# Kernel tuning notes

Hardware: AMD Instinct MI355X
Metric: run time of the kernel (lower is better)

## Reference

```python
import jax, jax.numpy as jnp
import numpy as np

EPS = 1e-8


def setup_inputs() -> dict:
    key = jax.random.key(0)
    k1, k2, k3, k4 = jax.random.split(key, 4)
    N, Cin, Cout, S, DHW, K = 4, 64, 64, 512, 48, 3
    return {
        "x": jax.random.normal(k1, (N, Cin, DHW, DHW, DHW), dtype=jnp.float32),
        "s": jax.random.normal(k2, (N, S), dtype=jnp.float32),
        "style_weight": jax.random.normal(k3, (Cin, S), dtype=jnp.float32) * (1.0 / np.sqrt(S)),
        "style_bias": jnp.ones((Cin,), dtype=jnp.float32),
        "weight": jax.random.normal(k4, (Cout, Cin, K, K, K), dtype=jnp.float32) * (1.0 / np.sqrt(Cin * K**3)),
        "bias": jnp.zeros((Cout,), dtype=jnp.float32),
    }


def reference(x, s, style_weight, style_bias, weight, bias):
    N, Cin = x.shape[0], x.shape[1]
    Cout = weight.shape[0]
    # style modulation: per-sample per-input-channel scale
    style = s @ style_weight.T + style_bias                      # [N, Cin]
    w = weight[None] * style[:, None, :, None, None, None]       # [N, Cout, Cin, k, k, k]
    # demodulation over fan-in dims (Cin, k, k, k)
    w = w * jax.lax.rsqrt(jnp.sum(w * w, axis=(2, 3, 4, 5), keepdims=True) + EPS)
    w = w.reshape(N * Cout, Cin, *w.shape[3:])                   # grouped kernel
    xg = x.reshape(1, N * Cin, *x.shape[2:])
    y = jax.lax.conv_general_dilated(
        xg, w,
        window_strides=(1, 1, 1),
        padding='VALID',
        feature_group_count=N,
        dimension_numbers=('NCDHW', 'OIDHW', 'NCDHW'),
    )                                                            # [1, N*Cout, D', H', W']
    y = y.reshape(N, Cout, *y.shape[2:])
    return y + bias[None, :, None, None, None]
```

## Files before the change

kernel.cpp:

```cpp
#include <hip/hip_runtime.h>

typedef float f32x4 __attribute__((ext_vector_type(4)));
typedef short bf16x8 __attribute__((ext_vector_type(8)));

#define AS1 __attribute__((address_space(1)))
#define AS3 __attribute__((address_space(3)))

__device__ __forceinline__ void gl16(const void* g, void* l) {
  __builtin_amdgcn_global_load_lds((const AS1 unsigned int*)g,
                                   (AS3 unsigned int*)l, 16, 0, 0);
}

__device__ __forceinline__ unsigned short f2bf(float f) {
  unsigned u = __float_as_uint(f);
  u = u + 0x7FFFu + ((u >> 16) & 1u);
  return (unsigned short)(u >> 16);
}

__global__ __launch_bounds__(256) void k_style(const float* __restrict__ s,
                                               const float* __restrict__ sw,
                                               const float* __restrict__ sb,
                                               float* __restrict__ style) {
  int t = threadIdx.x;
  int n = t >> 6, i = t & 63;
  float acc = sb[i];
  const float* sp = s + n * 512;
  const float* wp = sw + i * 512;
  for (int k = 0; k < 512; ++k) acc += sp[k] * wp[k];
  style[t] = acc;
}

__global__ __launch_bounds__(256) void k_wmod(const float* __restrict__ weight,
                                              const float* __restrict__ style,
                                              unsigned short* __restrict__ wm) {
  int o = blockIdx.x, n = blockIdx.y, t = threadIdx.x;
  int lane = t & 63, wv = t >> 6;
  const float* wp = weight + o * 1728;
  const float* st = style + n * 64;
  float v[7];
  float ss = 0.f;
#pragma unroll
  for (int j = 0; j < 7; ++j) {
    int idx = t + j * 256;
    float w = 0.f;
    if (idx < 1728) {
      int i = idx / 27;
      w = wp[idx] * st[i];
    }
    v[j] = w;
    ss += w * w;
  }
#pragma unroll
  for (int off = 32; off > 0; off >>= 1) ss += __shfl_down(ss, off);
  __shared__ float red[4];
  if (lane == 0) red[wv] = ss;
  __syncthreads();
  float total = red[0] + red[1] + red[2] + red[3];
  float dm = 1.0f / sqrtf(total + 1e-8f);
#pragma unroll
  for (int j = 0; j < 7; ++j) {
    int idx = t + j * 256;
    if (idx < 1728) {
      int i = idx / 27, k = idx - i * 27;
      int g = (n * 27 + k) * 64 + o;
      wm[g * 64 + (((i >> 3) ^ (o & 7)) << 3) + (i & 7)] = f2bf(v[j] * dm);
    }
  }
}

__global__ __launch_bounds__(256) void k_xpose(const float* __restrict__ x,
                                               unsigned short* __restrict__ xT) {
  __shared__ unsigned tile[128][33];
  int n = blockIdx.y;
  int p0 = blockIdx.x * 128;
  int t = threadIdx.x;
  int wv = t >> 6, lane = t & 63;
  const float* xb = x + (size_t)n * 64 * 110592 + p0;
#pragma unroll
  for (int c = 0; c < 8; ++c) {
    int i2 = c * 4 + wv;
    int i = i2 * 2;
    int pl = lane * 2;
    const float* r0 = xb + (size_t)i * 110592 + pl;
    const float* r1 = r0 + 110592;
    float2 a = *(const float2*)r0;
    float2 b = *(const float2*)r1;
    tile[pl][i2]     = (unsigned)f2bf(a.x) | ((unsigned)f2bf(b.x) << 16);
    tile[pl + 1][i2] = (unsigned)f2bf(a.y) | ((unsigned)f2bf(b.y) << 16);
  }
  __syncthreads();
  uint4* dst = (uint4*)xT;
#pragma unroll
  for (int c = 0; c < 4; ++c) {
    int pl = (t >> 3) + c * 32;
    int r = t & 7;
    uint4 u;
    u.x = tile[pl][r * 4 + 0];
    u.y = tile[pl][r * 4 + 1];
    u.z = tile[pl][r * 4 + 2];
    u.w = tile[pl][r * 4 + 3];
    int R = n * 110592 + p0 + pl;
    dst[(size_t)R * 8 + (r ^ (pl & 7))] = u;
  }
}

__global__ __launch_bounds__(256) void k_conv(const unsigned short* __restrict__ xT,
                                              const unsigned short* __restrict__ wm,
                                              const float* __restrict__ bias,
                                              float* __restrict__ out) {
  __shared__ uint4 Bl4[46080 / 16];
  __shared__ uint4 Al4[2][8192 / 16];
  char* Bl = (char*)Bl4;

  int bid = blockIdx.x;
  int orig = (bid & 7) * 207 + (bid >> 3);
  int n = orig / 414;
  int pb = orig - n * 414;
  int p0 = pb * 256;

  int t = threadIdx.x;
  int lane = t & 63, wv = t >> 6;
  int l15 = lane & 15, lhi = lane >> 4;
  f32x4 acc[4][4] = {};

  const char* xb = (const char*)xT + ((size_t)(n * 110592 + p0)) * 128;
  const char* wb = (const char*)wm + (size_t)n * 27 * 8192;

  {
    const char* ap = wb;
    gl16(ap + wv * 1024 + lane * 16, (char*)Al4[0] + wv * 1024);
    gl16(ap + (wv + 4) * 1024 + lane * 16, (char*)Al4[0] + (wv + 4) * 1024);
  }

#pragma unroll
  for (int kd = 0; kd < 3; ++kd) {
    const char* src = xb + (size_t)kd * (2304 * 128);
    for (int cc = wv; cc < 45; cc += 4)
      gl16(src + cc * 1024 + lane * 16, Bl + cc * 1024);
    asm volatile("s_waitcnt vmcnt(0)" ::: "memory");
    __builtin_amdgcn_s_barrier();
    __builtin_amdgcn_sched_barrier(0);

#pragma unroll
    for (int tap = 0; tap < 9; ++tap) {
      const int s = kd * 9 + tap;
      const int cur = s & 1;
      if (s + 1 < 27) {
        const char* ap = wb + (size_t)(s + 1) * 8192;
        gl16(ap + wv * 1024 + lane * 16, (char*)Al4[cur ^ 1] + wv * 1024);
        gl16(ap + (wv + 4) * 1024 + lane * 16, (char*)Al4[cur ^ 1] + (wv + 4) * 1024);
      }
      const int kh = tap / 3, kw = tap - kh * 3;
      const int rbase = wv * 64 + kh * 48 + kw;
      const char* Alc = (const char*)Al4[cur];
#pragma unroll
      for (int ih = 0; ih < 2; ++ih) {
        int c = lhi + ih * 4;
        bf16x8 a[4], b[4];
#pragma unroll
        for (int m = 0; m < 4; ++m) {
          int orow = m * 16 + l15;
          a[m] = *(const bf16x8*)(Alc + orow * 128 + ((c ^ (orow & 7)) << 4));
        }
#pragma unroll
        for (int q = 0; q < 4; ++q) {
          int r = rbase + q * 16 + l15;
          b[q] = *(const bf16x8*)(Bl + r * 128 + ((c ^ (r & 7)) << 4));
        }
        __builtin_amdgcn_s_setprio(1);
#pragma unroll
        for (int m = 0; m < 4; ++m)
#pragma unroll
          for (int q = 0; q < 4; ++q)
            acc[m][q] = __builtin_amdgcn_mfma_f32_16x16x32_bf16(a[m], b[q], acc[m][q], 0, 0, 0);
        __builtin_amdgcn_s_setprio(0);
      }
      asm volatile("s_waitcnt vmcnt(0)" ::: "memory");
      __builtin_amdgcn_s_barrier();
      __builtin_amdgcn_sched_barrier(0);
    }
  }

  float bv[4][4];
#pragma unroll
  for (int m = 0; m < 4; ++m)
#pragma unroll
    for (int r = 0; r < 4; ++r) bv[m][r] = bias[m * 16 + lhi * 4 + r];

  float* ob = out + (size_t)n * 64 * 97336;
#pragma unroll
  for (int q = 0; q < 4; ++q) {
    int p = p0 + wv * 64 + q * 16 + l15;
    int d = p / 2304;
    int rem = p - d * 2304;
    int h = rem / 48;
    int w = rem - h * 48;
    if (h < 46 && w < 46) {
      int base = d * 2116 + h * 46 + w;
#pragma unroll
      for (int m = 0; m < 4; ++m)
#pragma unroll
        for (int r = 0; r < 4; ++r) {
          int o = m * 16 + lhi * 4 + r;
          ob[(size_t)o * 97336 + base] = acc[m][q][r] + bv[m][r];
        }
    }
  }
}

extern "C" void kernel_launch(void* const* d_in, const int* in_sizes, int n_in,
                              void* d_out, int out_size, void* d_ws, size_t ws_size,
                              hipStream_t stream) {
  const float* x    = (const float*)d_in[0];
  const float* s    = (const float*)d_in[1];
  const float* sw   = (const float*)d_in[2];
  const float* sb   = (const float*)d_in[3];
  const float* wt   = (const float*)d_in[4];
  const float* bias = (const float*)d_in[5];
  float* out = (float*)d_out;

  float* style          = (float*)d_ws;
  unsigned short* wm    = (unsigned short*)((char*)d_ws + 1024);
  unsigned short* xT    = (unsigned short*)((char*)d_ws + 1024 + 884736);

  hipLaunchKernelGGL(k_style, dim3(1), dim3(256), 0, stream, s, sw, sb, style);
  hipLaunchKernelGGL(k_wmod, dim3(64, 4), dim3(256), 0, stream, wt, style, wm);
  hipLaunchKernelGGL(k_xpose, dim3(864, 4), dim3(256), 0, stream, x, xT);
  hipLaunchKernelGGL(k_conv, dim3(1656), dim3(256), 0, stream, xT, wm, bias, out);
}
```

Measured before the change: 154.8 us.

## Load modulated weights directly into registers, dropping LDS staging and per-tap barriers

The per-tap weight tile is no longer staged through double-buffered LDS with global_load_lds. Each lane now loads its A fragments straight from global memory into registers, with a register ping-pong between aA and aB. This removes 27 per-tap waitcnt plus barrier pairs, keeping only the barriers around each kd input-slab reload, and frees 16KB of LDS. In exchange it adds about 64 VGPRs for the two A register sets and issues global loads with little latency hiding beyond one tap ahead, which may cut occupancy or stall on global latency.

```diff
diff --git a/kernel.cpp b/kernel.cpp
--- a/kernel.cpp
+++ b/kernel.cpp
@@ -109,7 +109,6 @@
                                               const float* __restrict__ bias,
                                               float* __restrict__ out) {
   __shared__ uint4 Bl4[46080 / 16];
-  __shared__ uint4 Al4[2][8192 / 16];
   char* Bl = (char*)Bl4;
 
   int bid = blockIdx.x;
@@ -126,60 +125,63 @@
   const char* xb = (const char*)xT + ((size_t)(n * 110592 + p0)) * 128;
   const char* wb = (const char*)wm + (size_t)n * 27 * 8192;
 
-  {
-    const char* ap = wb;
-    gl16(ap + wv * 1024 + lane * 16, (char*)Al4[0] + wv * 1024);
-    gl16(ap + (wv + 4) * 1024 + lane * 16, (char*)Al4[0] + (wv + 4) * 1024);
-  }
+  int aoff[8];
+#pragma unroll
+  for (int m = 0; m < 4; ++m)
+#pragma unroll
+    for (int ih = 0; ih < 2; ++ih) {
+      int orow = m * 16 + l15;
+      int c = lhi + ih * 4;
+      aoff[m * 2 + ih] = orow * 128 + ((c ^ (orow & 7)) << 4);
+    }
+
+  bf16x8 aA[8], aB[8];
+#pragma unroll
+  for (int j = 0; j < 8; ++j) aA[j] = *(const bf16x8*)(wb + aoff[j]);
+
+#define TAP(CUR, NXT, S, TP)                                                   \
+  do {                                                                         \
+    if ((S) + 1 < 27) {                                                        \
+      const char* ap_ = wb + (size_t)((S) + 1) * 8192;                         \
+      _Pragma("unroll") for (int j = 0; j < 8; ++j)                            \
+          NXT[j] = *(const bf16x8*)(ap_ + aoff[j]);                            \
+    }                                                                          \
+    __builtin_amdgcn_sched_barrier(0);                                         \
+    const int kh_ = (TP) / 3, kw_ = (TP) % 3;                                  \
+    const int rbase_ = wv * 64 + kh_ * 48 + kw_;                               \
+    _Pragma("unroll") for (int ih = 0; ih < 2; ++ih) {                         \
+      int c_ = lhi + ih * 4;                                                   \
+      bf16x8 b_[4];                                                            \
+      _Pragma("unroll") for (int q = 0; q < 4; ++q) {                          \
+        int r_ = rbase_ + q * 16 + l15;                                        \
+        b_[q] = *(const bf16x8*)(Bl + r_ * 128 + ((c_ ^ (r_ & 7)) << 4));      \
+      }                                                                        \
+      __builtin_amdgcn_s_setprio(1);                                           \
+      _Pragma("unroll") for (int m = 0; m < 4; ++m)                            \
+          _Pragma("unroll") for (int q = 0; q < 4; ++q)                        \
+              acc[m][q] = __builtin_amdgcn_mfma_f32_16x16x32_bf16(             \
+                  CUR[m * 2 + ih], b_[q], acc[m][q], 0, 0, 0);                 \
+      __builtin_amdgcn_s_setprio(0);                                           \
+    }                                                                          \
+  } while (0)
 
 #pragma unroll
   for (int kd = 0; kd < 3; ++kd) {
+    if (kd) __builtin_amdgcn_s_barrier();
     const char* src = xb + (size_t)kd * (2304 * 128);
     for (int cc = wv; cc < 45; cc += 4)
       gl16(src + cc * 1024 + lane * 16, Bl + cc * 1024);
     asm volatile("s_waitcnt vmcnt(0)" ::: "memory");
     __builtin_amdgcn_s_barrier();
     __builtin_amdgcn_sched_barrier(0);
-
-#pragma unroll
-    for (int tap = 0; tap < 9; ++tap) {
-      const int s = kd * 9 + tap;
-      const int cur = s & 1;
-      if (s + 1 < 27) {
-        const char* ap = wb + (size_t)(s + 1) * 8192;
-        gl16(ap + wv * 1024 + lane * 16, (char*)Al4[cur ^ 1] + wv * 1024);
-        gl16(ap + (wv + 4) * 1024 + lane * 16, (char*)Al4[cur ^ 1] + (wv + 4) * 1024);
-      }
-      const int kh = tap / 3, kw = tap - kh * 3;
-      const int rbase = wv * 64 + kh * 48 + kw;
-      const char* Alc = (const char*)Al4[cur];
-#pragma unroll
-      for (int ih = 0; ih < 2; ++ih) {
-        int c = lhi + ih * 4;
-        bf16x8 a[4], b[4];
-#pragma unroll
-        for (int m = 0; m < 4; ++m) {
-          int orow = m * 16 + l15;
-          a[m] = *(const bf16x8*)(Alc + orow * 128 + ((c ^ (orow & 7)) << 4));
-        }
-#pragma unroll
-        for (int q = 0; q < 4; ++q) {
-          int r = rbase + q * 16 + l15;
-          b[q] = *(const bf16x8*)(Bl + r * 128 + ((c ^ (r & 7)) << 4));
-        }
-        __builtin_amdgcn_s_setprio(1);
-#pragma unroll
-        for (int m = 0; m < 4; ++m)
-#pragma unroll
-          for (int q = 0; q < 4; ++q)
-            acc[m][q] = __builtin_amdgcn_mfma_f32_16x16x32_bf16(a[m], b[q], acc[m][q], 0, 0, 0);
-        __builtin_amdgcn_s_setprio(0);
-      }
-      asm volatile("s_waitcnt vmcnt(0)" ::: "memory");
-      __builtin_amdgcn_s_barrier();
-      __builtin_amdgcn_sched_barrier(0);
-    }
-  }
+#pragma unroll
+    for (int tp = 0; tp < 9; ++tp) {
+      const int s = kd * 9 + tp;
+      if ((s & 1) == 0) TAP(aA, aB, s, tp);
+      else              TAP(aB, aA, s, tp);
+    }
+  }
+#undef TAP
 
   float bv[4][4];
 #pragma unroll
```

New measurement: 150.8 us. 2.6% less time.
